# Optimization experiments

Measured on AMD Instinct MI355X. Metric: run time of the kernel, lower is better.

Reference implementation:

```python
import jax, jax.numpy as jnp
import numpy as np

N_NODES = 100000
N_EDGES = 1600000
IN_CH, HID_CH, OUT_CH = 64, 64, 16
N_REL = 8


def setup_inputs() -> dict:
    key = jax.random.key(0)
    ks = jax.random.split(key, 10)
    x = jax.random.normal(ks[0], (N_NODES, IN_CH), dtype=jnp.float32)
    edge_index = jax.random.randint(ks[1], (2, N_EDGES), 0, N_NODES, dtype=jnp.int64)
    edge_type = jax.random.randint(ks[2], (N_EDGES,), 0, N_REL, dtype=jnp.int64)
    # RGCNConv params: per-relation weight, root weight, bias (Glorot-ish scale)
    def glorot(k, shape):
        fan = shape[-2] + shape[-1]
        return jax.random.normal(k, shape, dtype=jnp.float32) * jnp.sqrt(2.0 / fan)
    W1 = glorot(ks[3], (N_REL, IN_CH, HID_CH))
    root1 = glorot(ks[4], (IN_CH, HID_CH))
    b1 = jnp.zeros((HID_CH,), dtype=jnp.float32)
    W2 = glorot(ks[5], (N_REL, HID_CH, OUT_CH))
    root2 = glorot(ks[6], (HID_CH, OUT_CH))
    b2 = jnp.zeros((OUT_CH,), dtype=jnp.float32)
    return {"x": x, "edge_index": edge_index, "edge_type": edge_type,
            "W1": W1, "root1": root1, "b1": b1,
            "W2": W2, "root2": root2, "b2": b2}


def rgcn_conv(x, src, dst, edge_type, W_rel, W_root, bias):
    """PyG RGCNConv: out_i = x_i @ W_root + b + sum_r mean_{j in N_r(i)} x_j @ W_r.
    Mean is linear, so aggregate raw features per relation, then transform."""
    n = x.shape[0]
    xs = x[src]  # [E, F] gathered source features (hot memory-bound op)
    out = x @ W_root + bias
    for r in range(W_rel.shape[0]):  # small fixed relation count
        mask = (edge_type == r).astype(x.dtype)  # [E]
        agg = jax.ops.segment_sum(xs * mask[:, None], dst, num_segments=n)  # [N, F]
        cnt = jax.ops.segment_sum(mask, dst, num_segments=n)  # [N]
        agg = agg / jnp.clip(cnt, 1.0)[:, None]  # mean aggr; 0 when no edges
        out = out + agg @ W_rel[r]
    return out


def reference(x, edge_index, edge_type, W1, root1, b1, W2, root2, b2):
    src, dst = edge_index[0], edge_index[1]
    h = rgcn_conv(x, src, dst, edge_type, W1, root1, b1)
    h = jax.nn.relu(h)
    h = rgcn_conv(h, src, dst, edge_type, W2, root2, b2)
    # global_mean_pool with a single graph: mean over nodes -> [1, out]
    g = jnp.mean(h, axis=0, keepdims=True)
    return jax.nn.log_softmax(g, axis=1)
```

## Files before the change

### kernel.cpp

```cpp
#include <hip/hip_runtime.h>
#include <hip/hip_bf16.h>


#define CH 64
#define BK_EDGES 2048
#define CAP 12288
#define RPT 12
#define KB 128
#define KRB 1024

typedef __attribute__((ext_vector_type(8))) short short8;
typedef __attribute__((ext_vector_type(4))) float f32x4;
typedef __attribute__((ext_vector_type(2))) float f32x2;

__device__ inline ushort f2bf(float f) {
    unsigned b = __float_as_uint(f);
    unsigned r = (b + 0x7FFFu + ((b >> 16) & 1u)) >> 16;
    return (ushort)r;
}
__device__ inline float bf2f(ushort u) {
    return __uint_as_float(((unsigned)u) << 16);
}

__device__ inline void acc8fp8(float* a, uint2 w, float m) {
    f32x2 p;
    p = __builtin_amdgcn_cvt_pk_f32_fp8(w.x, 0); a[0] += m * p.x; a[1] += m * p.y;
    p = __builtin_amdgcn_cvt_pk_f32_fp8(w.x, 1); a[2] += m * p.x; a[3] += m * p.y;
    p = __builtin_amdgcn_cvt_pk_f32_fp8(w.y, 0); a[4] += m * p.x; a[5] += m * p.y;
    p = __builtin_amdgcn_cvt_pk_f32_fp8(w.y, 1); a[6] += m * p.x; a[7] += m * p.y;
}

__device__ inline short8 dec8fp8(uint2 w) {
    float f[8];
    f32x2 p;
    p = __builtin_amdgcn_cvt_pk_f32_fp8(w.x, 0); f[0] = p.x; f[1] = p.y;
    p = __builtin_amdgcn_cvt_pk_f32_fp8(w.x, 1); f[2] = p.x; f[3] = p.y;
    p = __builtin_amdgcn_cvt_pk_f32_fp8(w.y, 0); f[4] = p.x; f[5] = p.y;
    p = __builtin_amdgcn_cvt_pk_f32_fp8(w.y, 1); f[6] = p.x; f[7] = p.y;
    short8 r;
    #pragma unroll
    for (int k = 0; k < 8; ++k) r[k] = (short)f2bf(f[k]);
    return r;
}


__global__ __launch_bounds__(256) void prep_kernel(
    const int* __restrict__ src, const int* __restrict__ dst,
    const int* __restrict__ etype,
    int* __restrict__ gBucketCnt, int2* __restrict__ bucket_buf,
    int E, int N)
{
    __shared__ int s_k[BK_EDGES];
    __shared__ int s_y[BK_EDGES];
    __shared__ int hist[256], scanv[256], lcur[256], bstart[256], gbase[256];
    const int t = threadIdx.x;
    const int bid = blockIdx.x;

    const int e0 = bid * BK_EDGES;
    const int cnt = min(BK_EDGES, E - e0);

    hist[t] = 0;
    __syncthreads();

    int myb[8], myk[8], myy[8];
    #pragma unroll
    for (int i = 0; i < 8; ++i) {
        int li = t + i * 256;
        if (li < cnt) {
            int e = e0 + li;
            int r = etype[e];
            int k = r * N + dst[e];
            myk[i] = k;
            myy[i] = (r << 17) | src[e];
            myb[i] = k >> 12;
            atomicAdd(&hist[myb[i]], 1);
        } else myb[i] = -1;
    }
    __syncthreads();

    int v = hist[t];
    scanv[t] = v;
    __syncthreads();
    for (int off = 1; off < 256; off <<= 1) {
        int u = (t >= off) ? scanv[t - off] : 0;
        __syncthreads();
        scanv[t] += u;
        __syncthreads();
    }
    int excl = scanv[t] - v;
    bstart[t] = excl;
    lcur[t] = excl;
    __syncthreads();

    #pragma unroll
    for (int i = 0; i < 8; ++i) {
        if (myb[i] >= 0) {
            int p = atomicAdd(&lcur[myb[i]], 1);
            s_k[p] = myk[i];
            s_y[p] = myy[i];
        }
    }
    __syncthreads();

    if (v > 0) gbase[t] = atomicAdd(&gBucketCnt[t], v);
    __syncthreads();

    for (int p = t; p < cnt; p += 256) {
        int k = s_k[p];
        int b = k >> 12;
        int gp = gbase[b] + (p - bstart[b]);
        if (gp < CAP)
            bucket_buf[(size_t)b * CAP + gp] = make_int2(k, s_y[p]);
    }
}


__global__ __launch_bounds__(1024) void build_kernel(
    const int2* __restrict__ bucket_buf, const int* __restrict__ gBucketCnt,
    int* __restrict__ rowptr, float* __restrict__ inv,
    int* __restrict__ perm,
    const float* __restrict__ x, const float* __restrict__ W1,
    const float* __restrict__ root1,
    unsigned char* __restrict__ xq, ushort* __restrict__ wf,
    float* __restrict__ kappa, int nkey,
    int N, int nbuk, int nXbf)
{
    __shared__ int hist[4096];
    __shared__ int cur[4096];
    __shared__ int part[1024];
    const int t = threadIdx.x;
    const int bid = blockIdx.x;

    if (bid >= nbuk) {
        int cb = bid - nbuk;
        if (cb < nXbf) {
            int i = cb * 1024 + t;
            if (i < N * CH / 4) {
                float4 v = ((const float4*)x)[i];
                int p8 = __builtin_amdgcn_cvt_pk_fp8_f32(v.x, v.y, 0, 0);
                p8 = __builtin_amdgcn_cvt_pk_fp8_f32(v.z, v.w, p8, 1);
                ((unsigned int*)xq)[i] = (unsigned int)p8;
            }
        } else {
            int idx = (cb - nXbf) * 1024 + t;
            if (idx < 9 * 2 * 4 * 64 * 8) {
                int j    = idx & 7;
                int lane = (idx >> 3) & 63;
                int ct   = (idx >> 9) & 3;
                int ks   = (idx >> 11) & 1;
                int rel  = idx >> 12;
                int k = ks * 32 + (lane >> 4) * 8 + j;
                int n = ct * 16 + (lane & 15);
                float v = (rel < 8) ? W1[((size_t)rel * 64 + k) * 64 + n]
                                    : root1[(size_t)k * 64 + n];
                wf[idx] = f2bf(v);
            }
        }
        return;
    }

    const int b = bid;
    const int nb = min(gBucketCnt[b], CAP);
    const int2* rec = bucket_buf + (size_t)b * CAP;

    for (int i = b * 1024 + t; i < nkey; i += nbuk * 1024)
        kappa[i] = 0.0f;

    int rk[RPT], ry[RPT];
    #pragma unroll
    for (int i = 0; i < RPT; ++i) {
        int j = t + i * 1024;
        if (j < nb) { int2 v = rec[j]; rk[i] = v.x; ry[i] = v.y; }
        else        { rk[i] = -1; ry[i] = 0; }
    }

    int bc = (t < 256) ? gBucketCnt[t] : 0;
    part[t] = bc;
    __syncthreads();
    for (int off = 1; off < 1024; off <<= 1) {
        int u = (t >= off) ? part[t - off] : 0;
        __syncthreads();
        part[t] += u;
        __syncthreads();
    }
    __shared__ int baseS;
    if (t == b) baseS = part[t] - bc;
    __syncthreads();
    const int base = baseS;

    for (int i = t; i < 4096; i += 1024) hist[i] = 0;
    __syncthreads();
    #pragma unroll
    for (int i = 0; i < RPT; ++i)
        if (rk[i] >= 0) atomicAdd(&hist[rk[i] & 4095], 1);
    __syncthreads();

    const int i0 = t * 4;
    int h0 = hist[i0], h1 = hist[i0 + 1], h2 = hist[i0 + 2], h3 = hist[i0 + 3];
    int s = h0 + h1 + h2 + h3;
    part[t] = s;
    __syncthreads();
    for (int off = 1; off < 1024; off <<= 1) {
        int u = (t >= off) ? part[t - off] : 0;
        __syncthreads();
        part[t] += u;
        __syncthreads();
    }
    int run = base + part[t] - s;
    int hk[4] = {h0, h1, h2, h3};
    #pragma unroll
    for (int k = 0; k < 4; ++k) {
        cur[i0 + k] = run;
        rowptr[b * 4096 + i0 + k] = run;
        inv[b * 4096 + i0 + k] = 1.0f / (float)max(hk[k], 1);
        run += hk[k];
    }
    __syncthreads();

    #pragma unroll
    for (int i = 0; i < RPT; ++i) {
        if (rk[i] >= 0) {
            int pos = atomicAdd(&cur[rk[i] & 4095], 1);
            perm[pos] = ry[i] & 0x1FFFF;
        }
    }
}


__global__ __launch_bounds__(256) void rgcn1_fused_kernel(
    const int* __restrict__ rowptr, const int* __restrict__ perm,
    const float* __restrict__ inv,
    const unsigned char* __restrict__ xq,
    const ushort* __restrict__ wfrag, const float* __restrict__ b1,
    const int2* __restrict__ bucket_buf, const int* __restrict__ gBucketCnt,
    float* __restrict__ kappa,
    ushort* __restrict__ h, int N, int nbuk)
{
    if (blockIdx.x < KB) {
        for (int b = blockIdx.x; b < nbuk; b += KB) {
            const int nb = min(gBucketCnt[b], CAP);
            const int2* rec = bucket_buf + (size_t)b * CAP;
            for (int j = (int)threadIdx.x; j < nb; j += 256) {
                int2 v = rec[j];
                float iv = inv[v.x];
                unsafeAtomicAdd(&kappa[((v.y & 0x1FFFF) << 3) | (v.y >> 17)], iv);
            }
        }
        return;
    }

    __shared__ ushort Abuf[4][16 * 72];
    __shared__ int    rpS[4][144];
    __shared__ float  invS[4][128];
    const int widx = threadIdx.x >> 6;
    const int lane = threadIdx.x & 63;
    const int wid = ((blockIdx.x - KB) << 2) | widx;
    const int base = wid << 4;
    if (base >= N) return;

    const int m0 = lane & 15;
    const int q  = lane >> 4;
    const int sg = lane >> 3;
    const int cg = lane & 7;
    ushort* ab = Abuf[widx];
    int*    rpL = rpS[widx];
    float*  ivL = invS[widx];

    for (int i = lane; i < 136; i += 64) {
        int r = i / 17, mm = i - r * 17;
        rpL[i] = rowptr[(size_t)r * N + base + mm];
    }
    for (int i = lane; i < 128; i += 64)
        ivL[i] = inv[(size_t)(i >> 4) * N + base + (i & 15)];

    f32x4 acc4[4];
    #pragma unroll
    for (int ct = 0; ct < 4; ++ct) acc4[ct] = (f32x4)(0.0f);

    for (int r = 0; r < 8; ++r) {
        const int iA = r * 17 + sg;
        const int iB = iA + 8;
        int jA = rpL[iA], eA = rpL[iA + 1];
        int jB = rpL[iB], eB = rpL[iB + 1];
        float a[8] = {}, bacc[8] = {};
        int s0A = perm[(jA     < eA) ? jA     : 0];
        int s1A = perm[(jA + 1 < eA) ? jA + 1 : 0];
        int s0B = perm[(jB     < eB) ? jB     : 0];
        int s1B = perm[(jB + 1 < eB) ? jB + 1 : 0];
        while (jA < eA || jB < eB) {
            uint2 w0A = *(const uint2*)(xq + (size_t)s0A * CH + (cg << 3));
            uint2 w1A = *(const uint2*)(xq + (size_t)s1A * CH + (cg << 3));
            uint2 w0B = *(const uint2*)(xq + (size_t)s0B * CH + (cg << 3));
            uint2 w1B = *(const uint2*)(xq + (size_t)s1B * CH + (cg << 3));
            int t0A = perm[(jA + 2 < eA) ? jA + 2 : 0];
            int t1A = perm[(jA + 3 < eA) ? jA + 3 : 0];
            int t0B = perm[(jB + 2 < eB) ? jB + 2 : 0];
            int t1B = perm[(jB + 3 < eB) ? jB + 3 : 0];
            float m0A = (jA     < eA) ? 1.f : 0.f;
            float m1A = (jA + 1 < eA) ? 1.f : 0.f;
            float m0B = (jB     < eB) ? 1.f : 0.f;
            float m1B = (jB + 1 < eB) ? 1.f : 0.f;
            acc8fp8(a,    w0A, m0A);
            acc8fp8(a,    w1A, m1A);
            acc8fp8(bacc, w0B, m0B);
            acc8fp8(bacc, w1B, m1B);
            s0A = t0A; s1A = t1A; s0B = t0B; s1B = t1B;
            jA += 2; jB += 2;
        }
        const float ivA = ivL[(r << 4) | sg];
        const float ivB = ivL[(r << 4) | (8 + sg)];
        short8 oA, oB;
        #pragma unroll
        for (int k = 0; k < 8; ++k) {
            oA[k] = (short)f2bf(a[k] * ivA);
            oB[k] = (short)f2bf(bacc[k] * ivB);
        }
        *(short8*)&ab[sg * 72 + (cg << 3)]       = oA;
        *(short8*)&ab[(8 + sg) * 72 + (cg << 3)] = oB;

        #pragma unroll
        for (int s = 0; s < 2; ++s) {
            short8 av = *(short8*)&ab[m0 * 72 + s * 32 + q * 8];
            #pragma unroll
            for (int ct = 0; ct < 4; ++ct) {
                short8 bv = *(const short8*)&wfrag[(((size_t)(r * 2 + s) * 4 + ct) * 64 + lane) * 8];
                acc4[ct] = __builtin_amdgcn_mfma_f32_16x16x32_bf16(av, bv, acc4[ct], 0, 0, 0);
            }
        }
    }

    {
        int node = min(base + m0, N - 1);
        #pragma unroll
        for (int s = 0; s < 2; ++s) {
            uint2 wv = *(const uint2*)(xq + (size_t)node * CH + s * 32 + q * 8);
            short8 av = dec8fp8(wv);
            #pragma unroll
            for (int ct = 0; ct < 4; ++ct) {
                short8 bv = *(const short8*)&wfrag[(((size_t)(8 * 2 + s) * 4 + ct) * 64 + lane) * 8];
                acc4[ct] = __builtin_amdgcn_mfma_f32_16x16x32_bf16(av, bv, acc4[ct], 0, 0, 0);
            }
        }
    }

    #pragma unroll
    for (int ct = 0; ct < 4; ++ct) {
        int c = ct * 16 + m0;
        float bb = b1[c];
        #pragma unroll
        for (int v = 0; v < 4; ++v) {
            int node = base + q * 4 + v;
            if (node < N)
                h[(size_t)node * CH + c] = f2bf(fmaxf(acc4[ct][v] + bb, 0.f));
        }
    }
}


__global__ __launch_bounds__(256) void kred_kernel(
    const ushort* __restrict__ h, const float* __restrict__ kappa,
    float* __restrict__ partial, int N)
{
    const int lane = threadIdx.x & 63;
    const int w = threadIdx.x >> 6;
    int wave = (blockIdx.x << 2) | w;
    const int wstride = gridDim.x << 2;
    float racc[9] = {};
    for (int i = wave; i < N; i += wstride) {
        float hv = bf2f(h[(size_t)i * CH + lane]);
        #pragma unroll
        for (int r = 0; r < 8; ++r) racc[r] += hv * kappa[i * 8 + r];
        racc[8] += hv;
    }
    __shared__ float red[4][9][64];
    #pragma unroll
    for (int r = 0; r < 9; ++r) red[w][r][lane] = racc[r];
    __syncthreads();
    if (w == 0) {
        #pragma unroll
        for (int r = 0; r < 9; ++r) {
            float s4 = red[0][r][lane] + red[1][r][lane] + red[2][r][lane] + red[3][r][lane];
            partial[(size_t)blockIdx.x * 576 + r * 64 + lane] = s4;
        }
    }
}


__global__ __launch_bounds__(576) void kred2_kernel(
    const float* __restrict__ partial, float* __restrict__ sacc,
    int* __restrict__ done,
    const float* __restrict__ root2, const float* __restrict__ W2,
    const float* __restrict__ b2, float* __restrict__ out,
    float invN, int nblk)
{
    const int j = threadIdx.x;
    const int chunk = nblk >> 3;
    const int b0 = blockIdx.x * chunk;
    float s = 0.f;
    for (int b = b0; b < b0 + chunk; b += 4) {
        float v0 = partial[(size_t)b * 576 + j];
        float v1 = partial[(size_t)(b + 1) * 576 + j];
        float v2 = partial[(size_t)(b + 2) * 576 + j];
        float v3 = partial[(size_t)(b + 3) * 576 + j];
        s += (v0 + v1) + (v2 + v3);
    }
    unsafeAtomicAdd(&sacc[j], s);
    __threadfence();
    __syncthreads();
    __shared__ int tk;
    if (j == 0) tk = atomicAdd(done, 1);
    __syncthreads();
    if (tk != 7) return;
    __threadfence();

    __shared__ float g[16];
    if (j < 16) {
        const float* s0 = sacc + 512;
        float acc = 0.f;
        for (int c = 0; c < 64; ++c) acc += s0[c] * root2[c * 16 + j];
        for (int r = 0; r < 8; ++r) {
            const float* sr = sacc + r * 64;
            for (int c = 0; c < 64; ++c) acc += sr[c] * W2[(r * 64 + c) * 16 + j];
        }
        g[j] = acc * invN + b2[j];
    }
    __syncthreads();
    if (j < 16) {
        float m = -1e30f;
        for (int i = 0; i < 16; ++i) m = fmaxf(m, g[i]);
        float sm = 0.f;
        for (int i = 0; i < 16; ++i) sm += expf(g[i] - m);
        out[j] = g[j] - (m + logf(sm));
    }
}


extern "C" void kernel_launch(void* const* d_in, const int* in_sizes, int n_in,
                              void* d_out, int out_size, void* d_ws, size_t ws_size,
                              hipStream_t stream)
{
    const float* x     = (const float*)d_in[0];
    const int*   eidx  = (const int*)d_in[1];
    const int*   etype = (const int*)d_in[2];
    const float* W1    = (const float*)d_in[3];
    const float* root1 = (const float*)d_in[4];
    const float* b1    = (const float*)d_in[5];
    const float* W2    = (const float*)d_in[6];
    const float* root2 = (const float*)d_in[7];
    const float* b2    = (const float*)d_in[8];
    float* out = (float*)d_out;

    const int E = in_sizes[1] / 2;
    const int N = in_sizes[0] / CH;
    const int NKEY = N * 8;
    const int NBUK = (NKEY + 4095) / 4096;
    const int KSPACE = NBUK << 12;
    const int* srcI = eidx;
    const int* dstI = eidx + E;

    int* wsi = (int*)d_ws;
    int*   gBucketCnt = wsi;
    float* sacc       = (float*)(gBucketCnt + 256);
    int*   done       = (int*)(sacc + 576);
    float* kappa      = (float*)(done + 16);
    float* inv        = kappa + NKEY;
    int*   rowptr     = (int*)(inv + KSPACE);
    int*   perm       = rowptr + KSPACE + 16;
    size_t off = (size_t)((perm + E) - wsi);
    off = (off + 1) & ~(size_t)1;
    int2*  bucket_buf = (int2*)(wsi + off);
    off += (size_t)NBUK * CAP * 2;
    off = (off + 7) & ~(size_t)7;
    ushort* wfg = (ushort*)(wsi + off);
    unsigned char* xq = (unsigned char*)(wfg + 36864);
    ushort* h = (ushort*)(xq + (size_t)N * CH);
    float* partial = (float*)(h + (size_t)N * CH);

    hipMemsetAsync(d_ws, 0, (size_t)(256 + 576 + 16) * 4, stream);

    const int nBin = (E + BK_EDGES - 1) / BK_EDGES;
    prep_kernel<<<nBin, 256, 0, stream>>>(
        srcI, dstI, etype, gBucketCnt, bucket_buf, E, N);

    const int nXbf = (N * CH / 4 + 1023) / 1024;
    const int nWf  = (36864 + 1023) / 1024;
    build_kernel<<<NBUK + nXbf + nWf, 1024, 0, stream>>>(
        bucket_buf, gBucketCnt, rowptr, inv, perm,
        x, W1, root1, xq, wfg, kappa, NKEY, N, NBUK, nXbf);

    const int tiles = (N + 15) / 16;
    rgcn1_fused_kernel<<<KB + (tiles + 3) / 4, 256, 0, stream>>>(
        rowptr, perm, inv, xq, wfg, b1, bucket_buf, gBucketCnt, kappa,
        h, N, NBUK);

    kred_kernel<<<KRB, 256, 0, stream>>>(h, kappa, partial, N);
    kred2_kernel<<<8, 576, 0, stream>>>(partial, sacc, done,
                                        root2, W2, b2, out,
                                        1.0f / (float)N, KRB);
}
```

Before: 270.6 us.

## Replace kappa atomic scatter with second CSR gather over fp8 hidden features

Removes the per-edge atomic kappa accumulation and its zeroing, instead storing layer-1 output as fp8 and running a second gather kernel that sums per-relation neighbor means per block. The column sum of h is fused into the layer-1 kernel epilogue, and the final reduction reads the new partials. This avoids contended float atomics and the bf16 h round trip, at the cost of a second full random gather over the edge list and extra fp8 quantisation error on h.

```diff
diff --git a/kernel.cpp b/kernel.cpp
--- a/kernel.cpp
+++ b/kernel.cpp
@@ -6,8 +6,6 @@
 #define BK_EDGES 2048
 #define CAP 12288
 #define RPT 12
-#define KB 128
-#define KRB 1024
 
 typedef __attribute__((ext_vector_type(8))) short short8;
 typedef __attribute__((ext_vector_type(4))) float f32x4;
@@ -122,7 +120,6 @@
     const float* __restrict__ x, const float* __restrict__ W1,
     const float* __restrict__ root1,
     unsigned char* __restrict__ xq, ushort* __restrict__ wf,
-    float* __restrict__ kappa, int nkey,
     int N, int nbuk, int nXbf)
 {
     __shared__ int hist[4096];
@@ -163,9 +160,6 @@
     const int nb = min(gBucketCnt[b], CAP);
     const int2* rec = bucket_buf + (size_t)b * CAP;
 
-    for (int i = b * 1024 + t; i < nkey; i += nbuk * 1024)
-        kappa[i] = 0.0f;
-
     int rk[RPT], ry[RPT];
     #pragma unroll
     for (int i = 0; i < RPT; ++i) {
@@ -232,31 +226,18 @@
     const float* __restrict__ inv,
     const unsigned char* __restrict__ xq,
     const ushort* __restrict__ wfrag, const float* __restrict__ b1,
-    const int2* __restrict__ bucket_buf, const int* __restrict__ gBucketCnt,
-    float* __restrict__ kappa,
-    ushort* __restrict__ h, int N, int nbuk)
+    unsigned char* __restrict__ hq, float* __restrict__ hsum_partial,
+    int N)
 {
-    if (blockIdx.x < KB) {
-        for (int b = blockIdx.x; b < nbuk; b += KB) {
-            const int nb = min(gBucketCnt[b], CAP);
-            const int2* rec = bucket_buf + (size_t)b * CAP;
-            for (int j = (int)threadIdx.x; j < nb; j += 256) {
-                int2 v = rec[j];
-                float iv = inv[v.x];
-                unsafeAtomicAdd(&kappa[((v.y & 0x1FFFF) << 3) | (v.y >> 17)], iv);
-            }
-        }
-        return;
-    }
-
     __shared__ ushort Abuf[4][16 * 72];
     __shared__ int    rpS[4][144];
     __shared__ float  invS[4][128];
+    __shared__ float  hsumS[4][64];
     const int widx = threadIdx.x >> 6;
     const int lane = threadIdx.x & 63;
-    const int wid = ((blockIdx.x - KB) << 2) | widx;
+    const int wid = (blockIdx.x << 2) | widx;
     const int base = wid << 4;
-    if (base >= N) return;
+    const bool active = base < N;
 
     const int m0 = lane & 15;
     const int q  = lane >> 4;
@@ -266,143 +247,236 @@
     int*    rpL = rpS[widx];
     float*  ivL = invS[widx];
 
-    for (int i = lane; i < 136; i += 64) {
-        int r = i / 17, mm = i - r * 17;
-        rpL[i] = rowptr[(size_t)r * N + base + mm];
-    }
-    for (int i = lane; i < 128; i += 64)
-        ivL[i] = inv[(size_t)(i >> 4) * N + base + (i & 15)];
-
     f32x4 acc4[4];
     #pragma unroll
     for (int ct = 0; ct < 4; ++ct) acc4[ct] = (f32x4)(0.0f);
 
+    if (active) {
+        for (int i = lane; i < 136; i += 64) {
+            int r = i / 17, mm = i - r * 17;
+            rpL[i] = rowptr[(size_t)r * N + base + mm];
+        }
+        for (int i = lane; i < 128; i += 64)
+            ivL[i] = inv[(size_t)(i >> 4) * N + base + (i & 15)];
+
+        for (int r = 0; r < 8; ++r) {
+            const int iA = r * 17 + sg;
+            const int iB = iA + 8;
+            int jA = rpL[iA], eA = rpL[iA + 1];
+            int jB = rpL[iB], eB = rpL[iB + 1];
+            float a[8] = {}, bacc[8] = {};
+            int s0A = perm[(jA     < eA) ? jA     : 0];
+            int s1A = perm[(jA + 1 < eA) ? jA + 1 : 0];
+            int s0B = perm[(jB     < eB) ? jB     : 0];
+            int s1B = perm[(jB + 1 < eB) ? jB + 1 : 0];
+            while (jA < eA || jB < eB) {
+                uint2 w0A = *(const uint2*)(xq + (size_t)s0A * CH + (cg << 3));
+                uint2 w1A = *(const uint2*)(xq + (size_t)s1A * CH + (cg << 3));
+                uint2 w0B = *(const uint2*)(xq + (size_t)s0B * CH + (cg << 3));
+                uint2 w1B = *(const uint2*)(xq + (size_t)s1B * CH + (cg << 3));
+                int t0A = perm[(jA + 2 < eA) ? jA + 2 : 0];
+                int t1A = perm[(jA + 3 < eA) ? jA + 3 : 0];
+                int t0B = perm[(jB + 2 < eB) ? jB + 2 : 0];
+                int t1B = perm[(jB + 3 < eB) ? jB + 3 : 0];
+                float m0A = (jA     < eA) ? 1.f : 0.f;
+                float m1A = (jA + 1 < eA) ? 1.f : 0.f;
+                float m0B = (jB     < eB) ? 1.f : 0.f;
+                float m1B = (jB + 1 < eB) ? 1.f : 0.f;
+                acc8fp8(a,    w0A, m0A);
+                acc8fp8(a,    w1A, m1A);
+                acc8fp8(bacc, w0B, m0B);
+                acc8fp8(bacc, w1B, m1B);
+                s0A = t0A; s1A = t1A; s0B = t0B; s1B = t1B;
+                jA += 2; jB += 2;
+            }
+            const float ivA = ivL[(r << 4) | sg];
+            const float ivB = ivL[(r << 4) | (8 + sg)];
+            short8 oA, oB;
+            #pragma unroll
+            for (int k = 0; k < 8; ++k) {
+                oA[k] = (short)f2bf(a[k] * ivA);
+                oB[k] = (short)f2bf(bacc[k] * ivB);
+            }
+            *(short8*)&ab[sg * 72 + (cg << 3)]       = oA;
+            *(short8*)&ab[(8 + sg) * 72 + (cg << 3)] = oB;
+
+            #pragma unroll
+            for (int s = 0; s < 2; ++s) {
+                short8 av = *(short8*)&ab[m0 * 72 + s * 32 + q * 8];
+                #pragma unroll
+                for (int ct = 0; ct < 4; ++ct) {
+                    short8 bv = *(const short8*)&wfrag[(((size_t)(r * 2 + s) * 4 + ct) * 64 + lane) * 8];
+                    acc4[ct] = __builtin_amdgcn_mfma_f32_16x16x32_bf16(av, bv, acc4[ct], 0, 0, 0);
+                }
+            }
+        }
+
+        {
+            int node = min(base + m0, N - 1);
+            #pragma unroll
+            for (int s = 0; s < 2; ++s) {
+                uint2 wv = *(const uint2*)(xq + (size_t)node * CH + s * 32 + q * 8);
+                short8 av = dec8fp8(wv);
+                #pragma unroll
+                for (int ct = 0; ct < 4; ++ct) {
+                    short8 bv = *(const short8*)&wfrag[(((size_t)(8 * 2 + s) * 4 + ct) * 64 + lane) * 8];
+                    acc4[ct] = __builtin_amdgcn_mfma_f32_16x16x32_bf16(av, bv, acc4[ct], 0, 0, 0);
+                }
+            }
+        }
+
+        #pragma unroll
+        for (int ct = 0; ct < 4; ++ct) {
+            int c = ct * 16 + m0;
+            float bb = b1[c];
+            #pragma unroll
+            for (int v = 0; v < 4; ++v)
+                ab[(q * 4 + v) * 64 + c] = f2bf(fmaxf(acc4[ct][v] + bb, 0.f));
+        }
+
+        {
+            int row = lane >> 2, qt = lane & 3;
+            if (base + row < N) {
+                unsigned up[4];
+                #pragma unroll
+                for (int w = 0; w < 4; ++w) {
+                    int c0 = qt * 16 + w * 4;
+                    float f0 = bf2f(ab[row * 64 + c0 + 0]);
+                    float f1 = bf2f(ab[row * 64 + c0 + 1]);
+                    float f2 = bf2f(ab[row * 64 + c0 + 2]);
+                    float f3 = bf2f(ab[row * 64 + c0 + 3]);
+                    int u = __builtin_amdgcn_cvt_pk_fp8_f32(f0, f1, 0, 0);
+                    u = __builtin_amdgcn_cvt_pk_fp8_f32(f2, f3, u, 1);
+                    up[w] = (unsigned)u;
+                }
+                uint4 uv = make_uint4(up[0], up[1], up[2], up[3]);
+                *(uint4*)&hq[(size_t)(base + row) * CH + qt * 16] = uv;
+            }
+        }
+    }
+
+    float s = 0.f;
+    if (active) {
+        #pragma unroll
+        for (int row = 0; row < 16; ++row)
+            if (base + row < N) s += bf2f(ab[row * 64 + lane]);
+    }
+    hsumS[widx][lane] = s;
+    __syncthreads();
+    if (widx == 0)
+        hsum_partial[(size_t)blockIdx.x * 64 + lane] =
+            hsumS[0][lane] + hsumS[1][lane] + hsumS[2][lane] + hsumS[3][lane];
+}
+
+
+__global__ __launch_bounds__(256) void rgcn2_gather_kernel(
+    const int* __restrict__ rowptr, const int* __restrict__ perm,
+    const float* __restrict__ inv, const unsigned char* __restrict__ hq,
+    float* __restrict__ rel_partial, int N)
+{
+    __shared__ int    rpS[4][144];
+    __shared__ float  invS[4][128];
+    __shared__ float  relS[4][512];
+    const int widx = threadIdx.x >> 6;
+    const int lane = threadIdx.x & 63;
+    const int wid = (blockIdx.x << 2) | widx;
+    const int base = wid << 4;
+    const bool active = base < N;
+
+    const int sg = lane >> 3;
+    const int cg = lane & 7;
+    int*   rpL = rpS[widx];
+    float* ivL = invS[widx];
+
+    float racc[8][8];
+    #pragma unroll
+    for (int r = 0; r < 8; ++r)
+        #pragma unroll
+        for (int k = 0; k < 8; ++k) racc[r][k] = 0.f;
+
+    if (active) {
+        for (int i = lane; i < 136; i += 64) {
+            int r = i / 17, mm = i - r * 17;
+            rpL[i] = rowptr[(size_t)r * N + base + mm];
+        }
+        for (int i = lane; i < 128; i += 64)
+            ivL[i] = inv[(size_t)(i >> 4) * N + base + (i & 15)];
+
+        #pragma unroll
+        for (int r = 0; r < 8; ++r) {
+            const int iA = r * 17 + sg;
+            const int iB = iA + 8;
+            int jA = rpL[iA], eA = rpL[iA + 1];
+            int jB = rpL[iB], eB = rpL[iB + 1];
+            float a[8] = {}, bacc[8] = {};
+            int s0A = perm[(jA     < eA) ? jA     : 0];
+            int s1A = perm[(jA + 1 < eA) ? jA + 1 : 0];
+            int s0B = perm[(jB     < eB) ? jB     : 0];
+            int s1B = perm[(jB + 1 < eB) ? jB + 1 : 0];
+            while (jA < eA || jB < eB) {
+                uint2 w0A = *(const uint2*)(hq + (size_t)s0A * CH + (cg << 3));
+                uint2 w1A = *(const uint2*)(hq + (size_t)s1A * CH + (cg << 3));
+                uint2 w0B = *(const uint2*)(hq + (size_t)s0B * CH + (cg << 3));
+                uint2 w1B = *(const uint2*)(hq + (size_t)s1B * CH + (cg << 3));
+                int t0A = perm[(jA + 2 < eA) ? jA + 2 : 0];
+                int t1A = perm[(jA + 3 < eA) ? jA + 3 : 0];
+                int t0B = perm[(jB + 2 < eB) ? jB + 2 : 0];
+                int t1B = perm[(jB + 3 < eB) ? jB + 3 : 0];
+                float m0A = (jA     < eA) ? 1.f : 0.f;
+                float m1A = (jA + 1 < eA) ? 1.f : 0.f;
+                float m0B = (jB     < eB) ? 1.f : 0.f;
+                float m1B = (jB + 1 < eB) ? 1.f : 0.f;
+                acc8fp8(a,    w0A, m0A);
+                acc8fp8(a,    w1A, m1A);
+                acc8fp8(bacc, w0B, m0B);
+                acc8fp8(bacc, w1B, m1B);
+                s0A = t0A; s1A = t1A; s0B = t0B; s1B = t1B;
+                jA += 2; jB += 2;
+            }
+            const float ivA = ivL[(r << 4) | sg];
+            const float ivB = ivL[(r << 4) | (8 + sg)];
+            #pragma unroll
+            for (int k = 0; k < 8; ++k)
+                racc[r][k] += ivA * a[k] + ivB * bacc[k];
+        }
+    }
+
+    #pragma unroll
     for (int r = 0; r < 8; ++r) {
-        const int iA = r * 17 + sg;
-        const int iB = iA + 8;
-        int jA = rpL[iA], eA = rpL[iA + 1];
-        int jB = rpL[iB], eB = rpL[iB + 1];
-        float a[8] = {}, bacc[8] = {};
-        int s0A = perm[(jA     < eA) ? jA     : 0];
-        int s1A = perm[(jA + 1 < eA) ? jA + 1 : 0];
-        int s0B = perm[(jB     < eB) ? jB     : 0];
-        int s1B = perm[(jB + 1 < eB) ? jB + 1 : 0];
-        while (jA < eA || jB < eB) {
-            uint2 w0A = *(const uint2*)(xq + (size_t)s0A * CH + (cg << 3));
-            uint2 w1A = *(const uint2*)(xq + (size_t)s1A * CH + (cg << 3));
-            uint2 w0B = *(const uint2*)(xq + (size_t)s0B * CH + (cg << 3));
-            uint2 w1B = *(const uint2*)(xq + (size_t)s1B * CH + (cg << 3));
-            int t0A = perm[(jA + 2 < eA) ? jA + 2 : 0];
-            int t1A = perm[(jA + 3 < eA) ? jA + 3 : 0];
-            int t0B = perm[(jB + 2 < eB) ? jB + 2 : 0];
-            int t1B = perm[(jB + 3 < eB) ? jB + 3 : 0];
-            float m0A = (jA     < eA) ? 1.f : 0.f;
-            float m1A = (jA + 1 < eA) ? 1.f : 0.f;
-            float m0B = (jB     < eB) ? 1.f : 0.f;
-            float m1B = (jB + 1 < eB) ? 1.f : 0.f;
-            acc8fp8(a,    w0A, m0A);
-            acc8fp8(a,    w1A, m1A);
-            acc8fp8(bacc, w0B, m0B);
-            acc8fp8(bacc, w1B, m1B);
-            s0A = t0A; s1A = t1A; s0B = t0B; s1B = t1B;
-            jA += 2; jB += 2;
-        }
-        const float ivA = ivL[(r << 4) | sg];
-        const float ivB = ivL[(r << 4) | (8 + sg)];
-        short8 oA, oB;
         #pragma unroll
         for (int k = 0; k < 8; ++k) {
-            oA[k] = (short)f2bf(a[k] * ivA);
-            oB[k] = (short)f2bf(bacc[k] * ivB);
-        }
-        *(short8*)&ab[sg * 72 + (cg << 3)]       = oA;
-        *(short8*)&ab[(8 + sg) * 72 + (cg << 3)] = oB;
-
-        #pragma unroll
-        for (int s = 0; s < 2; ++s) {
-            short8 av = *(short8*)&ab[m0 * 72 + s * 32 + q * 8];
-            #pragma unroll
-            for (int ct = 0; ct < 4; ++ct) {
-                short8 bv = *(const short8*)&wfrag[(((size_t)(r * 2 + s) * 4 + ct) * 64 + lane) * 8];
-                acc4[ct] = __builtin_amdgcn_mfma_f32_16x16x32_bf16(av, bv, acc4[ct], 0, 0, 0);
-            }
-        }
-    }
-
-    {
-        int node = min(base + m0, N - 1);
-        #pragma unroll
-        for (int s = 0; s < 2; ++s) {
-            uint2 wv = *(const uint2*)(xq + (size_t)node * CH + s * 32 + q * 8);
-            short8 av = dec8fp8(wv);
-            #pragma unroll
-            for (int ct = 0; ct < 4; ++ct) {
-                short8 bv = *(const short8*)&wfrag[(((size_t)(8 * 2 + s) * 4 + ct) * 64 + lane) * 8];
-                acc4[ct] = __builtin_amdgcn_mfma_f32_16x16x32_bf16(av, bv, acc4[ct], 0, 0, 0);
-            }
-        }
-    }
-
-    #pragma unroll
-    for (int ct = 0; ct < 4; ++ct) {
-        int c = ct * 16 + m0;
-        float bb = b1[c];
-        #pragma unroll
-        for (int v = 0; v < 4; ++v) {
-            int node = base + q * 4 + v;
-            if (node < N)
-                h[(size_t)node * CH + c] = f2bf(fmaxf(acc4[ct][v] + bb, 0.f));
-        }
-    }
-}
-
-
-__global__ __launch_bounds__(256) void kred_kernel(
-    const ushort* __restrict__ h, const float* __restrict__ kappa,
-    float* __restrict__ partial, int N)
-{
-    const int lane = threadIdx.x & 63;
-    const int w = threadIdx.x >> 6;
-    int wave = (blockIdx.x << 2) | w;
-    const int wstride = gridDim.x << 2;
-    float racc[9] = {};
-    for (int i = wave; i < N; i += wstride) {
-        float hv = bf2f(h[(size_t)i * CH + lane]);
-        #pragma unroll
-        for (int r = 0; r < 8; ++r) racc[r] += hv * kappa[i * 8 + r];
-        racc[8] += hv;
-    }
-    __shared__ float red[4][9][64];
-    #pragma unroll
-    for (int r = 0; r < 9; ++r) red[w][r][lane] = racc[r];
-    __syncthreads();
-    if (w == 0) {
-        #pragma unroll
-        for (int r = 0; r < 9; ++r) {
-            float s4 = red[0][r][lane] + red[1][r][lane] + red[2][r][lane] + red[3][r][lane];
-            partial[(size_t)blockIdx.x * 576 + r * 64 + lane] = s4;
-        }
+            float v = racc[r][k];
+            v += __shfl_xor(v, 8);
+            v += __shfl_xor(v, 16);
+            v += __shfl_xor(v, 32);
+            if (sg == 0) relS[widx][r * 64 + cg * 8 + k] = v;
+        }
+    }
+    __syncthreads();
+    for (int idx = threadIdx.x; idx < 512; idx += 256) {
+        float v = relS[0][idx] + relS[1][idx] + relS[2][idx] + relS[3][idx];
+        rel_partial[(size_t)blockIdx.x * 512 + idx] = v;
     }
 }
 
 
 __global__ __launch_bounds__(576) void kred2_kernel(
-    const float* __restrict__ partial, float* __restrict__ sacc,
-    int* __restrict__ done,
+    const float* __restrict__ rel_partial, const float* __restrict__ hsum_partial,
+    float* __restrict__ sacc, int* __restrict__ done,
     const float* __restrict__ root2, const float* __restrict__ W2,
     const float* __restrict__ b2, float* __restrict__ out,
     float invN, int nblk)
 {
     const int j = threadIdx.x;
-    const int chunk = nblk >> 3;
+    const int chunk = (nblk + 7) >> 3;
     const int b0 = blockIdx.x * chunk;
+    const int b1e = min(b0 + chunk, nblk);
     float s = 0.f;
-    for (int b = b0; b < b0 + chunk; b += 4) {
-        float v0 = partial[(size_t)b * 576 + j];
-        float v1 = partial[(size_t)(b + 1) * 576 + j];
-        float v2 = partial[(size_t)(b + 2) * 576 + j];
-        float v3 = partial[(size_t)(b + 3) * 576 + j];
-        s += (v0 + v1) + (v2 + v3);
+    if (j < 512) {
+        for (int b = b0; b < b1e; ++b) s += rel_partial[(size_t)b * 512 + j];
+    } else {
+        int c = j - 512;
+        for (int b = b0; b < b1e; ++b) s += hsum_partial[(size_t)b * 64 + c];
     }
     unsafeAtomicAdd(&sacc[j], s);
     __threadfence();
@@ -457,13 +531,14 @@
     const int KSPACE = NBUK << 12;
     const int* srcI = eidx;
     const int* dstI = eidx + E;
+    const int tiles = (N + 15) / 16;
+    const int NBLK  = (tiles + 3) / 4;
 
     int* wsi = (int*)d_ws;
     int*   gBucketCnt = wsi;
     float* sacc       = (float*)(gBucketCnt + 256);
     int*   done       = (int*)(sacc + 576);
-    float* kappa      = (float*)(done + 16);
-    float* inv        = kappa + NKEY;
+    float* inv        = (float*)(done + 16);
     int*   rowptr     = (int*)(inv + KSPACE);
     int*   perm       = rowptr + KSPACE + 16;
     size_t off = (size_t)((perm + E) - wsi);
@@ -473,8 +548,9 @@
     off = (off + 7) & ~(size_t)7;
     ushort* wfg = (ushort*)(wsi + off);
     unsigned char* xq = (unsigned char*)(wfg + 36864);
-    ushort* h = (ushort*)(xq + (size_t)N * CH);
-    float* partial = (float*)(h + (size_t)N * CH);
+    unsigned char* hq = xq + (size_t)N * CH;
+    float* rel_partial  = (float*)(hq + (size_t)N * CH);
+    float* hsum_partial = rel_partial + (size_t)NBLK * 512;
 
     hipMemsetAsync(d_ws, 0, (size_t)(256 + 576 + 16) * 4, stream);
 
@@ -486,15 +562,15 @@
     const int nWf  = (36864 + 1023) / 1024;
     build_kernel<<<NBUK + nXbf + nWf, 1024, 0, stream>>>(
         bucket_buf, gBucketCnt, rowptr, inv, perm,
-        x, W1, root1, xq, wfg, kappa, NKEY, N, NBUK, nXbf);
-
-    const int tiles = (N + 15) / 16;
-    rgcn1_fused_kernel<<<KB + (tiles + 3) / 4, 256, 0, stream>>>(
-        rowptr, perm, inv, xq, wfg, b1, bucket_buf, gBucketCnt, kappa,
-        h, N, NBUK);
-
-    kred_kernel<<<KRB, 256, 0, stream>>>(h, kappa, partial, N);
-    kred2_kernel<<<8, 576, 0, stream>>>(partial, sacc, done,
+        x, W1, root1, xq, wfg, N, NBUK, nXbf);
+
+    rgcn1_fused_kernel<<<NBLK, 256, 0, stream>>>(
+        rowptr, perm, inv, xq, wfg, b1, hq, hsum_partial, N);
+
+    rgcn2_gather_kernel<<<NBLK, 256, 0, stream>>>(
+        rowptr, perm, inv, hq, rel_partial, N);
+
+    kred2_kernel<<<8, 576, 0, stream>>>(rel_partial, hsum_partial, sacc, done,
                                         root2, W2, b2, out,
-                                        1.0f / (float)N, KRB);
-}
+                                        1.0f / (float)N, NBLK);
+}
```

Measured after the change: 372.0 us. +37.4%, slower.
